# Kernel optimization log

Measured on AMD Instinct MI355X. Metric: run time of the kernel, lower is better.

Reference implementation:

```python
import jax, jax.numpy as jnp
import numpy as np

N = 8192
D_IN = 128
D_OUT = 64


def setup_inputs() -> dict:
    key = jax.random.key(0)
    k1, k2, k3 = jax.random.split(key, 3)
    features = jax.random.normal(k1, (N, D_IN), dtype=jnp.float32)
    # uniform [0,1) entries -> strictly positive row sums (degrees)
    adjacency_matrix = jax.random.uniform(k2, (N, N), dtype=jnp.float32)
    weight = jax.random.normal(k3, (D_IN, D_OUT), dtype=jnp.float32)
    return {"features": features, "adjacency_matrix": adjacency_matrix, "weight": weight}


def reference(features, adjacency_matrix, weight):
    # degree_matrix = diag(rowsum(A)); inverse(sqrt(diag(d))) == diag(d^{-1/2})
    deg = jnp.sum(adjacency_matrix, axis=1)            # [N]
    d_inv_sqrt = 1.0 / jnp.sqrt(deg)                   # [N]
    # D^{-1/2} A D^{-1/2} via broadcasting instead of dense diag matmuls
    norm_adj = d_inv_sqrt[:, None] * adjacency_matrix * d_inv_sqrt[None, :]  # [N,N]
    # (norm_adj @ X) @ W -- contract small dim last for efficiency
    h = norm_adj @ features                            # [N, D_IN]
    return jax.nn.relu(h @ weight)                     # [N, D_OUT]
```

## Files before the change

### kernel.cpp

```cpp
#include <hip/hip_runtime.h>

#define N_NODES 8192
#define D_IN    128
#define D_OUT   64

typedef __attribute__((ext_vector_type(8))) short short8;
typedef __attribute__((ext_vector_type(4))) float f32x4;

__device__ __forceinline__ short f2bf(float f) {
    unsigned u = __builtin_bit_cast(unsigned, f);
    u += 0x7fff + ((u >> 16) & 1);
    return (short)(u >> 16);
}

__global__ __launch_bounds__(256) void k_deg(const float* __restrict__ A,
                                             float* __restrict__ dis) {
    const int wave = threadIdx.x >> 6;
    const int lane = threadIdx.x & 63;
    const int row  = blockIdx.x * 4 + wave;
    const float4* Ar = (const float4*)(A + (size_t)row * N_NODES);
    float s = 0.f;
#pragma unroll
    for (int i = 0; i < 32; ++i) {
        float4 v = Ar[lane + 64 * i];
        s += (v.x + v.y) + (v.z + v.w);
    }
#pragma unroll
    for (int off = 32; off; off >>= 1) s += __shfl_down(s, off, 64);
    if (lane == 0) dis[row] = rsqrtf(s);
}

__global__ __launch_bounds__(256) void k_gpack(const float* __restrict__ X,
                                               const float* __restrict__ W,
                                               const float* __restrict__ dis,
                                               unsigned short* __restrict__ Gp) {
    __shared__ float Wl[D_IN * D_OUT];
    __shared__ float Xl[32 * 129];
    const int t = blockIdx.x, tid = threadIdx.x;

    const float4* W4 = (const float4*)W;
    float4* Wl4 = (float4*)Wl;
#pragma unroll
    for (int i = 0; i < 8; ++i) Wl4[tid + 256 * i] = W4[tid + 256 * i];
    const float4* X4 = (const float4*)(X + (size_t)t * 32 * D_IN);
#pragma unroll
    for (int i = 0; i < 4; ++i) {
        int idx = tid + 256 * i;
        float4 v = X4[idx];
        int r = idx >> 5, c = (idx & 31) * 4;
        float* dst = Xl + r * 129 + c;
        dst[0] = v.x; dst[1] = v.y; dst[2] = v.z; dst[3] = v.w;
    }
    __syncthreads();

    const int kl = tid & 31;
    const int nb = (tid >> 5) * 8;
    float acc[8] = {0.f, 0.f, 0.f, 0.f, 0.f, 0.f, 0.f, 0.f};
    const float* xr = Xl + kl * 129;
    for (int d = 0; d < D_IN; ++d) {
        float xv = xr[d];
        const float* wr = Wl + d * D_OUT + nb;
#pragma unroll
        for (int c = 0; c < 8; ++c) acc[c] += xv * wr[c];
    }
    const float scale = dis[t * 32 + kl];
    const int quad = kl >> 3, j = kl & 7;
#pragma unroll
    for (int c = 0; c < 8; ++c) {
        int n = nb + c;
        int u = n >> 4;
        int lanei = quad * 16 + (n & 15);
        Gp[(((size_t)t * 4 + u) * 64 + lanei) * 8 + j] = (unsigned short)f2bf(acc[c] * scale);
    }
}

__global__ __launch_bounds__(256) void k_spmm(const float* __restrict__ A,
                                              const unsigned short* __restrict__ Gp,
                                              float* __restrict__ h2) {
    const int lane = threadIdx.x & 63;
    const int wave = threadIdx.x >> 6;
    const int quad = lane >> 4;
    const int l15  = lane & 15;
    const int row  = blockIdx.x * 64 + wave * 16 + l15;
    const float* Ar = A + (size_t)row * N_NODES;
    const int kt0 = blockIdx.y * 32;

    f32x4 acc[4] = {};
    const short8* Gq = (const short8*)Gp;

    for (int kt = kt0; kt < kt0 + 32; ++kt) {
        const float4* pa = (const float4*)(Ar + kt * 32 + quad * 8);
        float4 a0 = pa[0], a1 = pa[1];
        short8 af;
        af[0] = f2bf(a0.x); af[1] = f2bf(a0.y); af[2] = f2bf(a0.z); af[3] = f2bf(a0.w);
        af[4] = f2bf(a1.x); af[5] = f2bf(a1.y); af[6] = f2bf(a1.z); af[7] = f2bf(a1.w);
        const short8* gb = Gq + (size_t)kt * 4 * 64 + lane;
#pragma unroll
        for (int u = 0; u < 4; ++u) {
            short8 bf = gb[u * 64];
            acc[u] = __builtin_amdgcn_mfma_f32_16x16x32_bf16(af, bf, acc[u], 0, 0, 0);
        }
    }
#pragma unroll
    for (int u = 0; u < 4; ++u) {
#pragma unroll
        for (int r = 0; r < 4; ++r) {
            int orow = blockIdx.x * 64 + wave * 16 + quad * 4 + r;
            int ocol = u * 16 + l15;
            atomicAdd(&h2[(size_t)orow * D_OUT + ocol], acc[u][r]);
        }
    }
}

__global__ __launch_bounds__(256) void k_out(const float* __restrict__ h2,
                                             const float* __restrict__ dis,
                                             float* __restrict__ out) {
    int idx = blockIdx.x * 256 + threadIdx.x;
    float4 v = ((const float4*)h2)[idx];
    float s = dis[idx >> 4];
    float4 o;
    o.x = fmaxf(v.x * s, 0.f);
    o.y = fmaxf(v.y * s, 0.f);
    o.z = fmaxf(v.z * s, 0.f);
    o.w = fmaxf(v.w * s, 0.f);
    ((float4*)out)[idx] = o;
}

extern "C" void kernel_launch(void* const* d_in, const int* in_sizes, int n_in,
                              void* d_out, int out_size, void* d_ws, size_t ws_size,
                              hipStream_t stream) {
    const float* X = (const float*)d_in[0];
    const float* A = (const float*)d_in[1];
    const float* W = (const float*)d_in[2];
    float* out = (float*)d_out;

    char* ws = (char*)d_ws;
    float*          dis = (float*)ws;
    unsigned short* Gp  = (unsigned short*)(ws + 32768);
    float*          h2  = (float*)(ws + 32768 + 1048576);

    k_deg  <<<N_NODES / 4, 256, 0, stream>>>(A, dis);
    k_gpack<<<N_NODES / 32, 256, 0, stream>>>(X, W, dis, Gp);
    hipMemsetAsync(h2, 0, (size_t)N_NODES * D_OUT * sizeof(float), stream);
    k_spmm <<<dim3(N_NODES / 64, 8), 256, 0, stream>>>(A, Gp, h2);
    k_out  <<<(N_NODES * D_OUT / 4) / 256, 256, 0, stream>>>(h2, dis, out);
}
```

Measured before the change: 424.5 us.

## Cast A to bf16 in degree pass and replace atomics with split-K partials

The degree kernel now also writes a bf16 copy of the adjacency matrix, so the matmul kernel streams half as many bytes and skips per-element conversion. Each wave now computes two 16-row tiles that share the same B fragments. Split-K results go to separate partial buffers, reduced in the output kernel, which removes the atomics and the memset. The cost is an extra 128MB write, a large workspace, and a reduction that reads 16 partial slices.

```diff
diff --git a/kernel.cpp b/kernel.cpp
--- a/kernel.cpp
+++ b/kernel.cpp
@@ -3,6 +3,7 @@
 #define N_NODES 8192
 #define D_IN    128
 #define D_OUT   64
+#define NSPLIT  16
 
 typedef __attribute__((ext_vector_type(8))) short short8;
 typedef __attribute__((ext_vector_type(4))) float f32x4;
@@ -12,18 +13,31 @@
     u += 0x7fff + ((u >> 16) & 1);
     return (short)(u >> 16);
 }
+__device__ __forceinline__ unsigned f2bf_pack(float lo, float hi) {
+    unsigned a = __builtin_bit_cast(unsigned, lo);
+    a += 0x7fff + ((a >> 16) & 1);
+    unsigned b = __builtin_bit_cast(unsigned, hi);
+    b += 0x7fff + ((b >> 16) & 1);
+    return (a >> 16) | (b & 0xffff0000u);
+}
 
 __global__ __launch_bounds__(256) void k_deg(const float* __restrict__ A,
-                                             float* __restrict__ dis) {
+                                             float* __restrict__ dis,
+                                             unsigned short* __restrict__ A16) {
     const int wave = threadIdx.x >> 6;
     const int lane = threadIdx.x & 63;
     const int row  = blockIdx.x * 4 + wave;
     const float4* Ar = (const float4*)(A + (size_t)row * N_NODES);
+    uint2* Aw = (uint2*)(A16 + (size_t)row * N_NODES);
     float s = 0.f;
 #pragma unroll
     for (int i = 0; i < 32; ++i) {
         float4 v = Ar[lane + 64 * i];
         s += (v.x + v.y) + (v.z + v.w);
+        uint2 p;
+        p.x = f2bf_pack(v.x, v.y);
+        p.y = f2bf_pack(v.z, v.w);
+        Aw[lane + 64 * i] = p;
     }
 #pragma unroll
     for (int off = 32; off; off >>= 1) s += __shfl_down(s, off, 64);
@@ -55,7 +69,7 @@
 
     const int kl = tid & 31;
     const int nb = (tid >> 5) * 8;
-    float acc[8] = {0.f, 0.f, 0.f, 0.f, 0.f, 0.f, 0.f, 0.f};
+    float acc[8] = {0.f,0.f,0.f,0.f,0.f,0.f,0.f,0.f};
     const float* xr = Xl + kl * 129;
     for (int d = 0; d < D_IN; ++d) {
         float xv = xr[d];
@@ -74,55 +88,63 @@
     }
 }
 
-__global__ __launch_bounds__(256) void k_spmm(const float* __restrict__ A,
+__global__ __launch_bounds__(256) void k_spmm(const unsigned short* __restrict__ A16,
                                               const unsigned short* __restrict__ Gp,
-                                              float* __restrict__ h2) {
+                                              float* __restrict__ partial) {
     const int lane = threadIdx.x & 63;
     const int wave = threadIdx.x >> 6;
     const int quad = lane >> 4;
     const int l15  = lane & 15;
-    const int row  = blockIdx.x * 64 + wave * 16 + l15;
-    const float* Ar = A + (size_t)row * N_NODES;
-    const int kt0 = blockIdx.y * 32;
+    const int rowbase = blockIdx.x * 128 + wave * 32;
 
-    f32x4 acc[4] = {};
-    const short8* Gq = (const short8*)Gp;
+    const short8* Ar0 = (const short8*)(A16 + (size_t)(rowbase + l15) * N_NODES);
+    const short8* Ar1 = (const short8*)(A16 + (size_t)(rowbase + 16 + l15) * N_NODES);
+    const short8* Gq  = (const short8*)Gp;
 
-    for (int kt = kt0; kt < kt0 + 32; ++kt) {
-        const float4* pa = (const float4*)(Ar + kt * 32 + quad * 8);
-        float4 a0 = pa[0], a1 = pa[1];
-        short8 af;
-        af[0] = f2bf(a0.x); af[1] = f2bf(a0.y); af[2] = f2bf(a0.z); af[3] = f2bf(a0.w);
-        af[4] = f2bf(a1.x); af[5] = f2bf(a1.y); af[6] = f2bf(a1.z); af[7] = f2bf(a1.w);
-        const short8* gb = Gq + (size_t)kt * 4 * 64 + lane;
+    const int kt0 = blockIdx.y * (N_NODES / 32 / NSPLIT);
+    f32x4 acc[2][4] = {};
+
+    for (int kt = kt0; kt < kt0 + (N_NODES / 32 / NSPLIT); ++kt) {
+        short8 a0 = Ar0[kt * 4 + quad];
+        short8 a1 = Ar1[kt * 4 + quad];
+        const short8* gb = Gq + (size_t)kt * 256 + lane;
 #pragma unroll
         for (int u = 0; u < 4; ++u) {
-            short8 bf = gb[u * 64];
-            acc[u] = __builtin_amdgcn_mfma_f32_16x16x32_bf16(af, bf, acc[u], 0, 0, 0);
+            short8 b = gb[u * 64];
+            acc[0][u] = __builtin_amdgcn_mfma_f32_16x16x32_bf16(a0, b, acc[0][u], 0, 0, 0);
+            acc[1][u] = __builtin_amdgcn_mfma_f32_16x16x32_bf16(a1, b, acc[1][u], 0, 0, 0);
         }
     }
+
+    float* P = partial + (size_t)blockIdx.y * (N_NODES * D_OUT);
 #pragma unroll
-    for (int u = 0; u < 4; ++u) {
+    for (int rt = 0; rt < 2; ++rt)
 #pragma unroll
-        for (int r = 0; r < 4; ++r) {
-            int orow = blockIdx.x * 64 + wave * 16 + quad * 4 + r;
-            int ocol = u * 16 + l15;
-            atomicAdd(&h2[(size_t)orow * D_OUT + ocol], acc[u][r]);
-        }
-    }
+        for (int u = 0; u < 4; ++u)
+#pragma unroll
+            for (int r = 0; r < 4; ++r) {
+                int gr = rowbase + rt * 16 + quad * 4 + r;
+                P[(size_t)gr * D_OUT + u * 16 + l15] = acc[rt][u][r];
+            }
 }
 
-__global__ __launch_bounds__(256) void k_out(const float* __restrict__ h2,
+__global__ __launch_bounds__(256) void k_out(const float* __restrict__ partial,
                                              const float* __restrict__ dis,
                                              float* __restrict__ out) {
-    int idx = blockIdx.x * 256 + threadIdx.x;
-    float4 v = ((const float4*)h2)[idx];
-    float s = dis[idx >> 4];
+    const int idx = blockIdx.x * 256 + threadIdx.x;
+    const float4* p4 = (const float4*)partial;
+    float4 s = p4[idx];
+#pragma unroll
+    for (int sp = 1; sp < NSPLIT; ++sp) {
+        float4 v = p4[idx + sp * (N_NODES * D_OUT / 4)];
+        s.x += v.x; s.y += v.y; s.z += v.z; s.w += v.w;
+    }
+    const float sc = dis[idx >> 4];
     float4 o;
-    o.x = fmaxf(v.x * s, 0.f);
-    o.y = fmaxf(v.y * s, 0.f);
-    o.z = fmaxf(v.z * s, 0.f);
-    o.w = fmaxf(v.w * s, 0.f);
+    o.x = fmaxf(s.x * sc, 0.f);
+    o.y = fmaxf(s.y * sc, 0.f);
+    o.z = fmaxf(s.z * sc, 0.f);
+    o.w = fmaxf(s.w * sc, 0.f);
     ((float4*)out)[idx] = o;
 }
 
@@ -135,13 +157,13 @@
     float* out = (float*)d_out;
 
     char* ws = (char*)d_ws;
-    float*          dis = (float*)ws;
-    unsigned short* Gp  = (unsigned short*)(ws + 32768);
-    float*          h2  = (float*)(ws + 32768 + 1048576);
+    float*          dis     = (float*)ws;
+    unsigned short* Gp      = (unsigned short*)(ws + (1u << 20));
+    unsigned short* A16     = (unsigned short*)(ws + (2u << 20));
+    float*          partial = (float*)(ws + (2u << 20) + ((size_t)128 << 20));
 
-    k_deg  <<<N_NODES / 4, 256, 0, stream>>>(A, dis);
+    k_deg  <<<N_NODES / 4, 256, 0, stream>>>(A, dis, A16);
     k_gpack<<<N_NODES / 32, 256, 0, stream>>>(X, W, dis, Gp);
-    hipMemsetAsync(h2, 0, (size_t)N_NODES * D_OUT * sizeof(float), stream);
-    k_spmm <<<dim3(N_NODES / 64, 8), 256, 0, stream>>>(A, Gp, h2);
-    k_out  <<<(N_NODES * D_OUT / 4) / 256, 256, 0, stream>>>(h2, dis, out);
+    k_spmm <<<dim3(N_NODES / 128, NSPLIT), 256, 0, stream>>>(A16, Gp, partial);
+    k_out  <<<(N_NODES * D_OUT / 4) / 256, 256, 0, stream>>>(partial, dis, out);
 }
```

New measurement: 434.1 us. +2.3%, slower.
